# Optimization experiments

Hardware: AMD Instinct MI355X
Metric: run time of the kernel (lower is better)

Reference implementation:

```python
import jax, jax.numpy as jnp
import numpy as np

N_NODES = 100000
N_EDGES = 1600000
IN_DIM = 16
HID = 128
N_LAYERS = 3
LN_EPS = 1e-5


def setup_inputs() -> dict:
    key = jax.random.key(0)
    ks = jax.random.split(key, 8)
    x = jax.random.normal(ks[0], (N_NODES, IN_DIM), dtype=jnp.float32)
    edge_index = jax.random.randint(ks[1], (2, N_EDGES), 0, N_NODES, dtype=jnp.int64)
    # input projection params
    W_in = jax.random.normal(ks[2], (IN_DIM, HID), dtype=jnp.float32) * (1.0 / np.sqrt(IN_DIM))
    b_in = jnp.zeros((HID,), dtype=jnp.float32)
    # stacked GCNConv weights [L, H, H] and biases [L, H]
    W_conv = jax.random.normal(ks[3], (N_LAYERS, HID, HID), dtype=jnp.float32) * (1.0 / np.sqrt(HID))
    b_conv = jnp.zeros((N_LAYERS, HID), dtype=jnp.float32)
    # LayerNorm params [L, H]
    ln_gamma = jnp.ones((N_LAYERS, HID), dtype=jnp.float32)
    ln_beta = jnp.zeros((N_LAYERS, HID), dtype=jnp.float32)
    return {"x": x, "edge_index": edge_index, "W_in": W_in, "b_in": b_in,
            "W_conv": W_conv, "b_conv": b_conv, "ln_gamma": ln_gamma, "ln_beta": ln_beta}


def _layer_norm(h, gamma, beta):
    mu = jnp.mean(h, axis=-1, keepdims=True)
    var = jnp.mean(jnp.square(h - mu), axis=-1, keepdims=True)
    return (h - mu) * jax.lax.rsqrt(var + LN_EPS) * gamma + beta


def reference(x, edge_index, W_in, b_in, W_conv, b_conv, ln_gamma, ln_beta):
    N = x.shape[0]
    loops = jnp.arange(N, dtype=edge_index.dtype)
    src = jnp.concatenate([edge_index[0], loops])  # add self-loops (GCNConv default)
    dst = jnp.concatenate([edge_index[1], loops])
    # symmetric normalization D^-1/2 (A+I) D^-1/2
    deg = jax.ops.segment_sum(jnp.ones(src.shape[0], dtype=x.dtype), dst, num_segments=N)
    dis = jax.lax.rsqrt(jnp.maximum(deg, 1.0))  # deg >= 1 with self-loops
    coef = (dis[src] * dis[dst])[:, None]  # [E+N, 1]
    h = x @ W_in + b_in  # input projection -> [N, HID]
    for l in range(N_LAYERS):
        h_prev = h
        m = h @ W_conv[l]  # transform then propagate (same math as GCNConv)
        agg = jax.ops.segment_sum(m[src] * coef, dst, num_segments=N) + b_conv[l]
        h = jax.nn.relu(_layer_norm(agg, ln_gamma[l], ln_beta[l]))
        if l > 0:  # residual only for i > 0, dims always match
            h = h + h_prev
    return h
```

## Files before the change

kernel.cpp:

```cpp
#include <hip/hip_runtime.h>
#include <hip/hip_bf16.h>
#include <hip/hip_fp16.h>

#define HID 128
#define BCHUNK 4096

typedef __attribute__((ext_vector_type(8))) short short8;
typedef __attribute__((ext_vector_type(4))) float f32x4;

__device__ __forceinline__ float ldf(const void* p, size_t i, int bf16f) {
    if (bf16f) {
        unsigned short u = ((const unsigned short*)p)[i];
        union { unsigned int x; float f; } v; v.x = ((unsigned int)u) << 16;
        return v.f;
    }
    return ((const float*)p)[i];
}
__device__ __forceinline__ int ld_idx(const void* p, size_t i, int i64f) {
    return i64f ? (int)((const long long*)p)[i] : ((const int*)p)[i];
}
__device__ __forceinline__ unsigned short f2bfu(float f) {
    __hip_bfloat16 h = __float2bfloat16(f);
    return *reinterpret_cast<unsigned short*>(&h);
}
__device__ __forceinline__ float bflo(unsigned int u) {
    union { unsigned int x; float f; } v; v.x = u << 16;
    return v.f;
}
__device__ __forceinline__ float bfhi(unsigned int u) {
    union { unsigned int x; float f; } v; v.x = u & 0xffff0000u;
    return v.f;
}

__global__ void k_init(const void* __restrict__ gamma, const void* __restrict__ ei,
                       int* flags, int* bkcur, int nbk) {
    int t = threadIdx.x;
    for (int i = t; i < nbk; i += 256) bkcur[i] = 0;
    if (t == 0) {
        unsigned int g0 = ((const unsigned int*)gamma)[0];
        flags[0] = (g0 != 0x3F800000u) ? 1 : 0;
        const unsigned int* e32 = (const unsigned int*)ei;
        int i64 = 1;
        for (int k = 0; k < 128; k++)
            if (e32[2 * k + 1] != 0u) { i64 = 0; break; }
        flags[1] = i64;
    }
}

__global__ __launch_bounds__(256) void k_bucket(const void* __restrict__ ei,
                                                int E, int N, int nbk, int cap,
                                                int* bkcur, unsigned* __restrict__ bdata,
                                                const int* __restrict__ flags) {
    __shared__ int hist[512], base[512];
    int i64 = flags[1];
    int t = threadIdx.x;
    for (int i = t; i < nbk; i += 256) hist[i] = 0;
    __syncthreads();
    int e0 = blockIdx.x * BCHUNK;
    int ss[16], dd[16];
#pragma unroll
    for (int k = 0; k < 16; k++) {
        int e = e0 + k * 256 + t;
        dd[k] = -1;
        if (e < E) {
            int d = ld_idx(ei, (size_t)E + e, i64);
            int s = ld_idx(ei, e, i64);
            if ((unsigned)d < (unsigned)N && (unsigned)s < (unsigned)N) {
                dd[k] = d; ss[k] = s;
                atomicAdd(&hist[d >> 9], 1);
            }
        }
    }
    __syncthreads();
    for (int i = t; i < nbk; i += 256) {
        int c = hist[i];
        base[i] = c ? atomicAdd(&bkcur[i], c) : 0;
        hist[i] = 0;
    }
    __syncthreads();
#pragma unroll
    for (int k = 0; k < 16; k++) {
        if (dd[k] >= 0) {
            int b = dd[k] >> 9;
            int pos = base[b] + atomicAdd(&hist[b], 1);
            if (pos < cap)
                bdata[(size_t)b * cap + pos] =
                    (unsigned)ss[k] | ((unsigned)(dd[k] & 511) << 17);
        }
    }
}

__global__ __launch_bounds__(256) void k_bfused(const int* __restrict__ bkcur,
                                                const unsigned* __restrict__ bdata,
                                                int cap, int* __restrict__ row_ptr,
                                                float* __restrict__ dis,
                                                int* __restrict__ csr_src,
                                                int N, int nbk) {
    __shared__ int hist[512];
    __shared__ int sb[256];
    __shared__ int lsum, bkbase;
    int b = blockIdx.x, t = threadIdx.x;
    int bv = (t < nbk) ? min(bkcur[t], cap) : 0;
    sb[t] = bv;
    __syncthreads();
    int acc = bv;
    for (int off = 1; off < 256; off <<= 1) {
        int x = (t >= off) ? sb[t - off] : 0;
        __syncthreads();
        acc += x; sb[t] = acc;
        __syncthreads();
    }
    if (t == b) bkbase = acc - bv;
    if (b == nbk - 1 && t == nbk - 1) row_ptr[N] = acc;
    for (int i = t; i < 512; i += 256) hist[i] = 0;
    __syncthreads();
    int cb = min(bkcur[b], cap);
    for (int k = t; k < cb; k += 256)
        atomicAdd(&hist[bdata[(size_t)b * cap + k] >> 17], 1);
    __syncthreads();
    int v0 = hist[t], v1 = hist[256 + t];
    int s0 = v0, s1 = v1;
    for (int off = 1; off < 256; off <<= 1) {
        int x0 = (t >= off) ? hist[t - off] : 0;
        int x1 = (t >= off) ? hist[256 + t - off] : 0;
        __syncthreads();
        s0 += x0; s1 += x1;
        hist[t] = s0; hist[256 + t] = s1;
        __syncthreads();
    }
    if (t == 255) lsum = s0;
    __syncthreads();
    int nbase = b << 9;
    int e0 = bkbase + s0 - v0;
    int e1 = bkbase + lsum + s1 - v1;
    if (nbase + t < N) {
        row_ptr[nbase + t] = e0;
        dis[nbase + t] = rsqrtf((float)(v0 + 1));
    }
    if (nbase + 256 + t < N) {
        row_ptr[nbase + 256 + t] = e1;
        dis[nbase + 256 + t] = rsqrtf((float)(v1 + 1));
    }
    __syncthreads();
    hist[t] = e0; hist[256 + t] = e1;
    __syncthreads();
    for (int k = t; k < cb; k += 256) {
        unsigned u = bdata[(size_t)b * cap + k];
        int j = atomicAdd(&hist[u >> 17], 1);
        csr_src[j] = (int)(u & 0x1FFFFu);
    }
}

__global__ void k_proj(const void* __restrict__ x, const void* __restrict__ Win,
                       const void* __restrict__ bin,
                       unsigned short* __restrict__ hb, int N,
                       const void* __restrict__ Wc, unsigned short* __restrict__ Wt,
                       const int* __restrict__ flags) {
    int bf = flags[0];
    int t = threadIdx.x;
    if (blockIdx.x >= N) {
        int i = blockIdx.x - N;
        int l = i >> 7, n = i & 127;
        float w = ldf(Wc, (size_t)l * 16384 + (size_t)t * 128 + n, bf);
        Wt[(size_t)l * 16384 + (size_t)n * 128 + t] = f2bfu(w);
        return;
    }
    int node = blockIdx.x;
    __shared__ float xs[16];
    if (t < 16) xs[t] = ldf(x, (size_t)node * 16 + t, bf);
    __syncthreads();
    float acc = ldf(bin, t, bf);
#pragma unroll
    for (int k = 0; k < 16; k++)
        acc += xs[k] * ldf(Win, (size_t)k * HID + t, bf);
    hb[(size_t)node * HID + t] = f2bfu(acc);
}

__global__ __launch_bounds__(256) void k_gemm(const unsigned short* __restrict__ hb,
                                              const unsigned short* __restrict__ Wt,
                                              const float* __restrict__ dis,
                                              unsigned short* __restrict__ m, int N,
                                              int ntiles) {
    int t = threadIdx.x;
    int wave = t >> 6, lane = t & 63;
    int quad = lane >> 4, n15 = lane & 15;
    short8 bfr[4][8];
#pragma unroll
    for (int kc = 0; kc < 4; kc++)
#pragma unroll
        for (int nt = 0; nt < 8; nt++)
            bfr[kc][nt] = *(const short8*)(Wt + (size_t)(nt * 16 + n15) * HID +
                                           kc * 32 + quad * 8);
    int wid = blockIdx.x * 4 + wave;
    int nwaves = gridDim.x * 4;
    for (int tile = wid; tile < ntiles; tile += nwaves) {
        int row0 = tile * 16;
        int node = row0 + n15;
        int arow = min(node, N - 1);
        const short8* ap = (const short8*)(hb + (size_t)arow * HID + quad * 8);
        short8 a0 = ap[0], a1 = ap[4], a2 = ap[8], a3 = ap[12];
        float dn = dis[arow];
        f32x4 acc[8] = {};
#pragma unroll
        for (int nt = 0; nt < 8; nt++) {
            acc[nt] = __builtin_amdgcn_mfma_f32_16x16x32_bf16(bfr[0][nt], a0, acc[nt], 0, 0, 0);
            acc[nt] = __builtin_amdgcn_mfma_f32_16x16x32_bf16(bfr[1][nt], a1, acc[nt], 0, 0, 0);
            acc[nt] = __builtin_amdgcn_mfma_f32_16x16x32_bf16(bfr[2][nt], a2, acc[nt], 0, 0, 0);
            acc[nt] = __builtin_amdgcn_mfma_f32_16x16x32_bf16(bfr[3][nt], a3, acc[nt], 0, 0, 0);
        }
        if (node < N) {
            unsigned short* mp = m + (size_t)node * HID + quad * 4;
#pragma unroll
            for (int nt = 0; nt < 8; nt++) {
                unsigned lo = (unsigned)f2bfu(acc[nt][0] * dn) |
                              ((unsigned)f2bfu(acc[nt][1] * dn) << 16);
                unsigned hi = (unsigned)f2bfu(acc[nt][2] * dn) |
                              ((unsigned)f2bfu(acc[nt][3] * dn) << 16);
                *(uint2*)(mp + nt * 16) = make_uint2(lo, hi);
            }
        }
    }
}

__global__ __launch_bounds__(256) void k_layer(
        const int* __restrict__ row_ptr, const int* __restrict__ csr_src,
        const unsigned int* __restrict__ m2, const float* __restrict__ dis,
        const void* __restrict__ bc, size_t boff,
        const void* __restrict__ lg, const void* __restrict__ lb, size_t goff,
        unsigned int* __restrict__ hb, void* __restrict__ out, int N,
        int res, int last, const int* __restrict__ flags) {
    int t = threadIdx.x, wave = t >> 6, lane = t & 63;
    int wid = blockIdx.x * 4 + wave;
    int nwaves = gridDim.x * 4;
    int bf = flags[0];
    float bb0 = ldf(bc, boff + 2 * lane, bf), bb1 = ldf(bc, boff + 2 * lane + 1, bf);
    float g0 = ldf(lg, goff + 2 * lane, bf), g1 = ldf(lg, goff + 2 * lane + 1, bf);
    float be0 = ldf(lb, goff + 2 * lane, bf), be1 = ldf(lb, goff + 2 * lane + 1, bf);
    unsigned lim = (unsigned)(N - 1);

    for (int node = wid; node < N; node += nwaves) {
        int nodeu = __builtin_amdgcn_readfirstlane(node);
        float dn = dis[nodeu];
        unsigned int ms = m2[(unsigned)(nodeu * 64) + lane];
        float v0 = bflo(ms), v1 = bfhi(ms);
        int begu = __builtin_amdgcn_readfirstlane(row_ptr[nodeu]);
        int endu = __builtin_amdgcn_readfirstlane(row_ptr[nodeu + 1]);
        float p0 = 0.f, p1 = 0.f, q0 = 0.f, q1 = 0.f, r0 = 0.f, r1 = 0.f;
        int j = begu;
        int c0 = 0, c1 = 0, c2 = 0, c3 = 0, c4 = 0, c5 = 0, c6 = 0, c7 = 0;
        if (j + 7 < endu) {
            c0 = csr_src[j];     c1 = csr_src[j + 1];
            c2 = csr_src[j + 2]; c3 = csr_src[j + 3];
            c4 = csr_src[j + 4]; c5 = csr_src[j + 5];
            c6 = csr_src[j + 6]; c7 = csr_src[j + 7];
        }
        while (j + 7 < endu) {
            unsigned int u0 = m2[(unsigned)(c0 * 64) + lane];
            unsigned int u1 = m2[(unsigned)(c1 * 64) + lane];
            unsigned int u2 = m2[(unsigned)(c2 * 64) + lane];
            unsigned int u3 = m2[(unsigned)(c3 * 64) + lane];
            unsigned int u4 = m2[(unsigned)(c4 * 64) + lane];
            unsigned int u5 = m2[(unsigned)(c5 * 64) + lane];
            unsigned int u6 = m2[(unsigned)(c6 * 64) + lane];
            unsigned int u7 = m2[(unsigned)(c7 * 64) + lane];
            int jn = j + 8;
            int pj = min(jn, max(endu - 8, begu));
            int n0 = csr_src[pj],     n1 = csr_src[pj + 1];
            int n2 = csr_src[pj + 2], n3 = csr_src[pj + 3];
            int n4 = csr_src[pj + 4], n5 = csr_src[pj + 5];
            int n6 = csr_src[pj + 6], n7 = csr_src[pj + 7];
            v0 += bflo(u0); v1 += bfhi(u0);
            p0 += bflo(u1); p1 += bfhi(u1);
            q0 += bflo(u2); q1 += bfhi(u2);
            r0 += bflo(u3); r1 += bfhi(u3);
            v0 += bflo(u4); v1 += bfhi(u4);
            p0 += bflo(u5); p1 += bfhi(u5);
            q0 += bflo(u6); q1 += bfhi(u6);
            r0 += bflo(u7); r1 += bfhi(u7);
            c0 = n0; c1 = n1; c2 = n2; c3 = n3;
            c4 = n4; c5 = n5; c6 = n6; c7 = n7;
            j = jn;
        }
        if (j < endu) {
            int s0 = (int)min((unsigned)csr_src[j],     lim);
            int s1 = (int)min((unsigned)csr_src[j + 1], lim);
            int s2 = (int)min((unsigned)csr_src[j + 2], lim);
            int s3 = (int)min((unsigned)csr_src[j + 3], lim);
            int s4 = (int)min((unsigned)csr_src[j + 4], lim);
            int s5 = (int)min((unsigned)csr_src[j + 5], lim);
            int s6 = (int)min((unsigned)csr_src[j + 6], lim);
            int s7 = (int)min((unsigned)csr_src[j + 7], lim);
            unsigned int u0 = m2[(unsigned)(s0 * 64) + lane];
            unsigned int u1 = m2[(unsigned)(s1 * 64) + lane];
            unsigned int u2 = m2[(unsigned)(s2 * 64) + lane];
            unsigned int u3 = m2[(unsigned)(s3 * 64) + lane];
            unsigned int u4 = m2[(unsigned)(s4 * 64) + lane];
            unsigned int u5 = m2[(unsigned)(s5 * 64) + lane];
            unsigned int u6 = m2[(unsigned)(s6 * 64) + lane];
            unsigned int u7 = m2[(unsigned)(s7 * 64) + lane];
            u1 = (j + 1 < endu) ? u1 : 0u;
            u2 = (j + 2 < endu) ? u2 : 0u;
            u3 = (j + 3 < endu) ? u3 : 0u;
            u4 = (j + 4 < endu) ? u4 : 0u;
            u5 = (j + 5 < endu) ? u5 : 0u;
            u6 = (j + 6 < endu) ? u6 : 0u;
            u7 = (j + 7 < endu) ? u7 : 0u;
            v0 += bflo(u0); v1 += bfhi(u0);
            p0 += bflo(u1); p1 += bfhi(u1);
            q0 += bflo(u2); q1 += bfhi(u2);
            r0 += bflo(u3); r1 += bfhi(u3);
            v0 += bflo(u4); v1 += bfhi(u4);
            p0 += bflo(u5); p1 += bfhi(u5);
            q0 += bflo(u6); q1 += bfhi(u6);
            r0 += bflo(u7); r1 += bfhi(u7);
        }
        v0 += p0 + q0 + r0;
        v1 += p1 + q1 + r1;
        v0 = bb0 + v0 * dn;
        v1 = bb1 + v1 * dn;
        float s1 = v0 + v1, s2 = v0 * v0 + v1 * v1;
#pragma unroll
        for (int o = 32; o; o >>= 1) {
            s1 += __shfl_down(s1, o);
            s2 += __shfl_down(s2, o);
        }
        float sum = __shfl(s1, 0), sq = __shfl(s2, 0);
        float mu = sum * (1.0f / HID);
        float var = sq * (1.0f / HID) - mu * mu;
        float r = rsqrtf(var + 1e-5f);
        float o0 = fmaxf((v0 - mu) * r * g0 + be0, 0.f);
        float o1 = fmaxf((v1 - mu) * r * g1 + be1, 0.f);
        size_t widx = (size_t)nodeu * 64 + lane;
        if (res) {
            unsigned int hp = hb[widx];
            o0 += bflo(hp);
            o1 += bfhi(hp);
        }
        unsigned int packed = (unsigned int)f2bfu(o0) | ((unsigned int)f2bfu(o1) << 16);
        hb[widx] = packed;
        if (last) {
            if (bf) ((unsigned int*)out)[widx] = packed;
            else {
                size_t base = (size_t)nodeu * HID + 2 * lane;
                *(float2*)&((float*)out)[base] = make_float2(o0, o1);
            }
        }
    }
}

extern "C" void kernel_launch(void* const* d_in, const int* in_sizes, int n_in,
                              void* d_out, int out_size, void* d_ws, size_t ws_size,
                              hipStream_t stream) {
    const void* x   = d_in[0];
    const void* ei  = d_in[1];
    const void* Win = d_in[2];
    const void* bin = d_in[3];
    const void* Wc  = d_in[4];
    const void* bc  = d_in[5];
    const void* lg  = d_in[6];
    const void* lb  = d_in[7];

    int N = in_sizes[0] / 16;
    int E = in_sizes[1] / 2;
    int nbk = (N + 511) >> 9;
    int cap = ((E / nbk) * 2 + 255) & ~255;

    char* ws = (char*)d_ws;
    size_t off = 0;
    auto alloc = [&](size_t bytes) {
        void* p = ws + off;
        off += (bytes + 255) / 256 * 256;
        return p;
    };
    int*            flags    = (int*)alloc(256);
    float*          dis      = (float*)alloc((size_t)N * 4);
    int*            row_ptr  = (int*)alloc(((size_t)N + 1) * 4);
    int*            bkcur    = (int*)alloc((size_t)nbk * 4);
    unsigned*       bdata    = (unsigned*)alloc((size_t)nbk * cap * 4);
    int*            csr_src  = (int*)alloc((size_t)E * 4 + 64);
    unsigned short* hb       = (unsigned short*)alloc((size_t)N * HID * 2);
    unsigned short* m        = (unsigned short*)alloc((size_t)N * HID * 2);
    unsigned short* Wt       = (unsigned short*)alloc((size_t)3 * HID * HID * 2);
    (void)ws_size;

    k_init<<<1, 256, 0, stream>>>(lg, ei, flags, bkcur, nbk);
    k_bucket<<<(E + BCHUNK - 1) / BCHUNK, 256, 0, stream>>>(ei, E, N, nbk, cap,
                                                            bkcur, bdata, flags);
    k_bfused<<<nbk, 256, 0, stream>>>(bkcur, bdata, cap, row_ptr, dis, csr_src,
                                      N, nbk);
    k_proj<<<N + 3 * HID, HID, 0, stream>>>(x, Win, bin, hb, N, Wc, Wt, flags);

    int ntiles = (N + 15) / 16;
    int lblocks = min((N + 3) / 4, 2048);
    for (int l = 0; l < 3; l++) {
        k_gemm<<<512, 256, 0, stream>>>(hb, Wt + (size_t)l * HID * HID, dis, m, N,
                                        ntiles);
        k_layer<<<lblocks, 256, 0, stream>>>(row_ptr, csr_src,
                                             (const unsigned int*)m, dis, bc,
                                             (size_t)l * HID, lg, lb, (size_t)l * HID,
                                             (unsigned int*)hb, d_out, N,
                                             l > 0, l == 2, flags);
    }
}
```

Measured before the change: 437.6 us.

## Restructure input projection, prefetch next GEMM tile, guard tail neighbor loads

Input projection now uses a persistent grid of 2048 blocks, one wave per node. Each lane keeps its W_in columns in registers and writes two bf16 values packed in one 32-bit store, replacing the earlier one-block-per-node launch that used shared memory and a barrier. The weight transpose is packed into 192 blocks of 256 threads. The GEMM kernel now software-prefetches the next tile's A rows and dis values while it computes the current tile, to hide load latency. The aggregation tail stops reading CSR entries past the row end and reuses the first source index instead, which avoids out-of-range index loads and extra scattered gathers.

After: 415.0 us, median of 2. 1.05x faster.

```diff
diff --git a/kernel.cpp b/kernel.cpp
--- a/kernel.cpp
+++ b/kernel.cpp
@@ -151,29 +151,43 @@
     }
 }
 
-__global__ void k_proj(const void* __restrict__ x, const void* __restrict__ Win,
-                       const void* __restrict__ bin,
-                       unsigned short* __restrict__ hb, int N,
+__global__ __launch_bounds__(256) void k_proj(const void* __restrict__ x,
+                       const void* __restrict__ Win, const void* __restrict__ bin,
+                       unsigned int* __restrict__ hb2, int N, int mblk,
                        const void* __restrict__ Wc, unsigned short* __restrict__ Wt,
                        const int* __restrict__ flags) {
     int bf = flags[0];
     int t = threadIdx.x;
-    if (blockIdx.x >= N) {
-        int i = blockIdx.x - N;
-        int l = i >> 7, n = i & 127;
-        float w = ldf(Wc, (size_t)l * 16384 + (size_t)t * 128 + n, bf);
-        Wt[(size_t)l * 16384 + (size_t)n * 128 + t] = f2bfu(w);
+    if (blockIdx.x >= mblk) {
+        int i = (blockIdx.x - mblk) * 256 + t;
+        int l = i >> 14, r = i & 16383;
+        int n = r >> 7, k = r & 127;
+        float w = ldf(Wc, (size_t)l * 16384 + (size_t)k * 128 + n, bf);
+        Wt[(size_t)l * 16384 + (size_t)n * 128 + k] = f2bfu(w);
         return;
     }
-    int node = blockIdx.x;
-    __shared__ float xs[16];
-    if (t < 16) xs[t] = ldf(x, (size_t)node * 16 + t, bf);
-    __syncthreads();
-    float acc = ldf(bin, t, bf);
-#pragma unroll
-    for (int k = 0; k < 16; k++)
-        acc += xs[k] * ldf(Win, (size_t)k * HID + t, bf);
-    hb[(size_t)node * HID + t] = f2bfu(acc);
+    int wave = t >> 6, lane = t & 63;
+    int wid = blockIdx.x * 4 + wave;
+    int nwaves = mblk * 4;
+    float w0[16], w1[16];
+#pragma unroll
+    for (int k = 0; k < 16; k++) {
+        w0[k] = ldf(Win, (size_t)k * HID + 2 * lane, bf);
+        w1[k] = ldf(Win, (size_t)k * HID + 2 * lane + 1, bf);
+    }
+    float b0 = ldf(bin, 2 * lane, bf), b1 = ldf(bin, 2 * lane + 1, bf);
+    for (int node = wid; node < N; node += nwaves) {
+        int nu = __builtin_amdgcn_readfirstlane(node);
+        float a0 = b0, a1 = b1;
+#pragma unroll
+        for (int k = 0; k < 16; k++) {
+            float xv = ldf(x, (size_t)nu * 16 + k, bf);
+            a0 += xv * w0[k];
+            a1 += xv * w1[k];
+        }
+        hb2[(unsigned)(nu * 64) + lane] =
+            (unsigned)f2bfu(a0) | ((unsigned)f2bfu(a1) << 16);
+    }
 }
 
 __global__ __launch_bounds__(256) void k_gemm(const unsigned short* __restrict__ hb,
@@ -193,13 +207,23 @@
                                            kc * 32 + quad * 8);
     int wid = blockIdx.x * 4 + wave;
     int nwaves = gridDim.x * 4;
-    for (int tile = wid; tile < ntiles; tile += nwaves) {
-        int row0 = tile * 16;
-        int node = row0 + n15;
-        int arow = min(node, N - 1);
-        const short8* ap = (const short8*)(hb + (size_t)arow * HID + quad * 8);
-        short8 a0 = ap[0], a1 = ap[4], a2 = ap[8], a3 = ap[12];
-        float dn = dis[arow];
+    int tile = wid;
+    if (tile >= ntiles) return;
+    int node = tile * 16 + n15;
+    int arow = min(node, N - 1);
+    const short8* ap = (const short8*)(hb + (size_t)arow * HID + quad * 8);
+    short8 a0 = ap[0], a1 = ap[4], a2 = ap[8], a3 = ap[12];
+    float dn = dis[arow];
+    while (true) {
+        int tile2 = tile + nwaves;
+        short8 c0, c1, c2, c3;
+        float dn2 = 0.f;
+        if (tile2 < ntiles) {
+            int ar2 = min(tile2 * 16 + n15, N - 1);
+            const short8* ap2 = (const short8*)(hb + (size_t)ar2 * HID + quad * 8);
+            c0 = ap2[0]; c1 = ap2[4]; c2 = ap2[8]; c3 = ap2[12];
+            dn2 = dis[ar2];
+        }
         f32x4 acc[8] = {};
 #pragma unroll
         for (int nt = 0; nt < 8; nt++) {
@@ -219,6 +243,10 @@
                 *(uint2*)(mp + nt * 16) = make_uint2(lo, hi);
             }
         }
+        if (tile2 >= ntiles) break;
+        a0 = c0; a1 = c1; a2 = c2; a3 = c3; dn = dn2;
+        tile = tile2;
+        node = tile * 16 + n15;
     }
 }
 
@@ -282,14 +310,14 @@
             j = jn;
         }
         if (j < endu) {
-            int s0 = (int)min((unsigned)csr_src[j],     lim);
-            int s1 = (int)min((unsigned)csr_src[j + 1], lim);
-            int s2 = (int)min((unsigned)csr_src[j + 2], lim);
-            int s3 = (int)min((unsigned)csr_src[j + 3], lim);
-            int s4 = (int)min((unsigned)csr_src[j + 4], lim);
-            int s5 = (int)min((unsigned)csr_src[j + 5], lim);
-            int s6 = (int)min((unsigned)csr_src[j + 6], lim);
-            int s7 = (int)min((unsigned)csr_src[j + 7], lim);
+            int s0 = (int)min((unsigned)csr_src[j], lim);
+            int s1 = (j + 1 < endu) ? (int)min((unsigned)csr_src[j + 1], lim) : s0;
+            int s2 = (j + 2 < endu) ? (int)min((unsigned)csr_src[j + 2], lim) : s0;
+            int s3 = (j + 3 < endu) ? (int)min((unsigned)csr_src[j + 3], lim) : s0;
+            int s4 = (j + 4 < endu) ? (int)min((unsigned)csr_src[j + 4], lim) : s0;
+            int s5 = (j + 5 < endu) ? (int)min((unsigned)csr_src[j + 5], lim) : s0;
+            int s6 = (j + 6 < endu) ? (int)min((unsigned)csr_src[j + 6], lim) : s0;
+            int s7 = (j + 7 < endu) ? (int)min((unsigned)csr_src[j + 7], lim) : s0;
             unsigned int u0 = m2[(unsigned)(s0 * 64) + lane];
             unsigned int u1 = m2[(unsigned)(s1 * 64) + lane];
             unsigned int u2 = m2[(unsigned)(s2 * 64) + lane];
@@ -388,7 +416,9 @@
                                                             bkcur, bdata, flags);
     k_bfused<<<nbk, 256, 0, stream>>>(bkcur, bdata, cap, row_ptr, dis, csr_src,
                                       N, nbk);
-    k_proj<<<N + 3 * HID, HID, 0, stream>>>(x, Win, bin, hb, N, Wc, Wt, flags);
+    int mblk = 2048;
+    k_proj<<<mblk + 192, 256, 0, stream>>>(x, Win, bin, (unsigned int*)hb, N, mblk,
+                                           Wc, Wt, flags);
 
     int ntiles = (N + 15) / 16;
     int lblocks = min((N + 3) / 4, 2048);
```
